# Optimization experiments

Measured on AMD Instinct MI355X. Metric: run time of the kernel, lower is better.

The kernel has to match this reference:

```python
import jax, jax.numpy as jnp
import numpy as np

B, N, D, C = 256, 200000, 128, 1000


def _l2_normalize(v, axis=-1, eps=1e-12):
    # matches torch F.normalize(p=2): v / max(||v||, eps)
    norm = jnp.sqrt(jnp.sum(v * v, axis=axis, keepdims=True))
    return v / jnp.maximum(norm, eps)


def setup_inputs() -> dict:
    key = jax.random.key(0)
    k1, k2, k3 = jax.random.split(key, 3)
    x = jax.random.normal(k1, (B, D), dtype=jnp.float32)
    index_embeddings = jax.random.normal(k2, (N, D), dtype=jnp.float32)
    class_labels = jax.random.randint(k3, (N,), 0, C, dtype=jnp.int32)
    return {
        "x": x,
        "index_embeddings": index_embeddings,
        "class_labels": class_labels,
        "num_classes": C,
    }


def reference(x, index_embeddings, class_labels, num_classes):
    # backbone output flattened -> embeddings [B, D]; L2-normalize (queries and index,
    # index normalization happens in add_index_data in the original module)
    emb = _l2_normalize(x)
    idx_emb = _l2_normalize(index_embeddings)
    # cosine similarities [B, N]
    similarities = jnp.einsum('bd,nd->bn', emb, idx_emb)
    # per-class max reduction (replaces Python loop over classes):
    # segment-max over the index dimension keyed by class_labels -> [B, num_classes]
    logits = jax.ops.segment_max(
        similarities.T, class_labels, num_segments=num_classes,
        indices_are_sorted=False,
    ).T
    return logits
```

## Files before the change

### kernel.cpp

```cpp
#include <hip/hip_runtime.h>
#include <hip/hip_bf16.h>
#include <stdint.h>

#define D_ 128
#define NB 64
#define KCH 4
#define NINF (-__builtin_inff())

typedef float f32x4 __attribute__((ext_vector_type(4)));
typedef short bf16x8 __attribute__((ext_vector_type(8)));

__device__ inline unsigned short f2bf(float f){
  unsigned x = __float_as_uint(f);
  return (unsigned short)((x + 0x7FFFu + ((x >> 16) & 1u)) >> 16);
}
__device__ inline unsigned packbf(float a, float b){
  return (unsigned)f2bf(a) | ((unsigned)f2bf(b) << 16);
}
__device__ inline unsigned fkey(float v){
  unsigned b = __float_as_uint(v);
  return (b & 0x80000000u) ? ~b : (b | 0x80000000u);
}

__global__ void k_norm_x(const float* __restrict__ x, unsigned short* __restrict__ xn){
  int row = blockIdx.x, lane = threadIdx.x;
  float2 v = reinterpret_cast<const float2*>(x + (size_t)row * D_)[lane];
  float ss = v.x * v.x + v.y * v.y;
  #pragma unroll
  for (int m = 1; m < 64; m <<= 1) ss += __shfl_xor(ss, m);
  float s = 1.0f / fmaxf(sqrtf(ss), 1e-12f);
  reinterpret_cast<unsigned*>(xn + (size_t)row * D_)[lane] = packbf(v.x * s, v.y * s);
}

__global__ void k_hist(const int* __restrict__ lab, unsigned* __restrict__ hist, int N, int C){
  __shared__ unsigned lh[1024];
  int t = threadIdx.x;
  for (int c = t; c < 1024; c += 256) lh[c] = 0;
  __syncthreads();
  for (int i = blockIdx.x * 256 + t; i < N; i += gridDim.x * 256)
    atomicAdd(&lh[lab[i]], 1u);
  __syncthreads();
  for (int c = t; c < C; c += 256) { unsigned v = lh[c]; if (v) atomicAdd(&hist[c], v); }
}

__global__ void k_scan(const unsigned* __restrict__ hist, unsigned* __restrict__ cursor, int C){
  __shared__ unsigned s[1024];
  int t = threadIdx.x;
  unsigned v = (t < C) ? hist[t] : 0u;
  s[t] = v; __syncthreads();
  for (int off = 1; off < 1024; off <<= 1){
    unsigned u = (t >= off) ? s[t - off] : 0u;
    __syncthreads();
    s[t] += u;
    __syncthreads();
  }
  if (t < C) cursor[t] = s[t] - v;
}

__global__ void k_scatter(const int* __restrict__ lab, unsigned* __restrict__ cursor,
                          int* __restrict__ perm, int* __restrict__ slab,
                          int* __restrict__ dstpos, int N){
  for (int i = blockIdx.x * 256 + threadIdx.x; i < N; i += gridDim.x * 256){
    int c = lab[i];
    unsigned pos = atomicAdd(&cursor[c], 1u);
    perm[pos] = i;
    slab[pos] = c;
    dstpos[i] = (int)pos;
  }
}

__global__ void k_init_out(unsigned* __restrict__ o, int n){
  int i = blockIdx.x * 256 + threadIdx.x;
  if (i < n) o[i] = 0x007FFFFFu;
}

__global__ void k_permnorm(const float* __restrict__ emb, const int* __restrict__ dstpos,
                           unsigned short* __restrict__ nrm, int N){
  int r = blockIdx.x * 64 + (threadIdx.x >> 2);
  if (r >= N) return;
  int j = threadIdx.x & 3;
  const f32x4* src = reinterpret_cast<const f32x4*>(emb + (size_t)r * D_ + j * 32);
  f32x4 v[8];
  #pragma unroll
  for (int i = 0; i < 8; i++) v[i] = src[i];
  float ss = 0.f;
  #pragma unroll
  for (int i = 0; i < 8; i++) ss += v[i][0]*v[i][0] + v[i][1]*v[i][1] + v[i][2]*v[i][2] + v[i][3]*v[i][3];
  ss += __shfl_xor(ss, 1); ss += __shfl_xor(ss, 2);
  float sc = 1.0f / fmaxf(sqrtf(ss), 1e-12f);
  int d = dstpos[r];
  unsigned o[16];
  #pragma unroll
  for (int i = 0; i < 8; i++){
    o[i*2]   = packbf(v[i][0]*sc, v[i][1]*sc);
    o[i*2+1] = packbf(v[i][2]*sc, v[i][3]*sc);
  }
  uint4* dst = reinterpret_cast<uint4*>(nrm + (size_t)d * D_ + j * 32);
  #pragma unroll
  for (int i = 0; i < 4; i++) dst[i] = make_uint4(o[i*4], o[i*4+1], o[i*4+2], o[i*4+3]);
}

__global__ __launch_bounds__(256, 3) void k_gemm(
    const unsigned short* __restrict__ nrm,
    const unsigned short* __restrict__ xn,
    const int* __restrict__ slab,
    unsigned* __restrict__ out_u,
    int nchunks, int N, int C){
  __shared__ __align__(16) unsigned short Ab[2][NB * D_];
  const int t = threadIdx.x;
  const int w = t >> 6, lane = t & 63, lr = lane & 15, lg = lane >> 4;

  const int cbeg = blockIdx.x * KCH;
  if (cbeg >= nchunks) return;
  int cend = cbeg + KCH; if (cend > nchunks) cend = nchunks;

  bf16x8 bf[4][4];
  #pragma unroll
  for (int ni = 0; ni < 4; ni++)
    #pragma unroll
    for (int kk = 0; kk < 4; kk++)
      bf[ni][kk] = *reinterpret_cast<const bf16x8*>(
          xn + (size_t)(w * 64 + ni * 16 + lr) * D_ + kk * 32 + lg * 8);

  const int c0 = slab[(size_t)cbeg * NB];
  float rT0=NINF, rT1=NINF, rT2=NINF, rT3=NINF, rT4=NINF, rT5=NINF, rT6=NINF, rT7=NINF;

  auto stageF = [&](int cn, int bb){
    const char* sb = (const char*)(nrm + (size_t)cn * NB * D_);
    char* lb = (char*)(&Ab[bb][0]);
    #pragma unroll
    for (int i = 0; i < 4; i++){
      int L = t * 16 + i * 4096;
      int row = L >> 8, s = (L >> 4) & 15;
      int so = row * 256 + ((s ^ (row & 7)) << 4);
      __builtin_amdgcn_global_load_lds(
          (const __attribute__((address_space(1))) unsigned int*)(sb + so),
          (__attribute__((address_space(3))) unsigned int*)(lb + L),
          16, 0, 0);
    }
  };

  stageF(cbeg, 0);

  for (int c = cbeg; c < cend; ++c){
    const int b = (c - cbeg) & 1;
    const int rowbase = c * NB;
    int rb = rowbase + lane;
    int myc = slab[rb < N ? rb : (N - 1)];
    int nx = __shfl_down(myc, 1);
    unsigned long long bmask = __ballot(lane < 63 && myc != nx);
    asm volatile("s_waitcnt vmcnt(0)" ::: "memory");
    if (c + 1 < cend) stageF(c + 1, b ^ 1);
    asm volatile("s_barrier" ::: "memory");

    f32x4 acc[4][4];
    #pragma unroll
    for (int mi = 0; mi < 4; mi++)
      #pragma unroll
      for (int ni = 0; ni < 4; ni++)
        acc[mi][ni] = (f32x4){0.f, 0.f, 0.f, 0.f};

    #pragma unroll
    for (int mi = 0; mi < 4; mi++){
      const int row = mi * 16 + lr;
      const char* rp = (const char*)(&Ab[b][0]) + row * 256;
      #pragma unroll
      for (int kk = 0; kk < 4; kk++){
        bf16x8 af = *reinterpret_cast<const bf16x8*>(rp + (((kk * 4 + lg) ^ (row & 7)) << 4));
        #pragma unroll
        for (int ni = 0; ni < 4; ni++)
          acc[mi][ni] = __builtin_amdgcn_mfma_f32_16x16x32_bf16(af, bf[ni][kk], acc[mi][ni], 0, 0, 0);
      }
    }

    int a = 0;
    unsigned long long mm = bmask;
    for (;;){
      int e = mm ? (__builtin_ctzll(mm) + 1) : 64;
      int cls = __shfl(myc, a);
      float m0=NINF, m1=NINF, m2=NINF, m3=NINF;
      #pragma unroll
      for (int mi = 0; mi < 4; mi++)
        #pragma unroll
        for (int rg = 0; rg < 4; rg++){
          int row = mi * 16 + lg * 4 + rg;
          bool in = (row >= a) && (row < e) && (rowbase + row < N);
          m0 = in ? fmaxf(m0, acc[mi][0][rg]) : m0;
          m1 = in ? fmaxf(m1, acc[mi][1][rg]) : m1;
          m2 = in ? fmaxf(m2, acc[mi][2][rg]) : m2;
          m3 = in ? fmaxf(m3, acc[mi][3][rg]) : m3;
        }
      m0 = fmaxf(m0, __shfl_xor(m0, 16)); m0 = fmaxf(m0, __shfl_xor(m0, 32));
      m1 = fmaxf(m1, __shfl_xor(m1, 16)); m1 = fmaxf(m1, __shfl_xor(m1, 32));
      m2 = fmaxf(m2, __shfl_xor(m2, 16)); m2 = fmaxf(m2, __shfl_xor(m2, 32));
      m3 = fmaxf(m3, __shfl_xor(m3, 16)); m3 = fmaxf(m3, __shfl_xor(m3, 32));
      float mv = (lg < 2) ? ((lg == 0) ? m0 : m1) : ((lg == 2) ? m2 : m3);
      int slot = cls - c0;
      switch (slot){
        case 0: rT0 = fmaxf(rT0, mv); break;
        case 1: rT1 = fmaxf(rT1, mv); break;
        case 2: rT2 = fmaxf(rT2, mv); break;
        case 3: rT3 = fmaxf(rT3, mv); break;
        case 4: rT4 = fmaxf(rT4, mv); break;
        case 5: rT5 = fmaxf(rT5, mv); break;
        case 6: rT6 = fmaxf(rT6, mv); break;
        case 7: rT7 = fmaxf(rT7, mv); break;
        default: atomicMax(&out_u[(size_t)t * C + cls], fkey(mv)); break;
      }
      if (e >= 64) break;
      a = e; mm &= mm - 1;
    }
    asm volatile("s_barrier" ::: "memory");
  }

  const size_t ob = (size_t)t * C;
  #define FLUSH(S_, V_) { int cls = c0 + S_; if (cls < C && V_ != NINF) atomicMax(&out_u[ob + cls], fkey(V_)); }
  FLUSH(0, rT0) FLUSH(1, rT1) FLUSH(2, rT2) FLUSH(3, rT3)
  FLUSH(4, rT4) FLUSH(5, rT5) FLUSH(6, rT6) FLUSH(7, rT7)
  #undef FLUSH
}

struct __align__(16) GSm {
  unsigned short A[NB * 136];
  float sims[16 * 257];
  float scale[NB];
  int rowid[NB];
  int clab[NB];
};

__global__ __launch_bounds__(256, 2) void k_gemm_gather(
    const float* __restrict__ emb, const unsigned short* __restrict__ xn,
    const int* __restrict__ perm, const int* __restrict__ slab,
    unsigned* __restrict__ out_u, int N, int C){
  __shared__ GSm sm;
  const int t = threadIdx.x;
  const int base = blockIdx.x * NB;
  if (t < NB){
    int p = base + t; if (p > N - 1) p = N - 1;
    sm.rowid[t] = perm[p];
    sm.clab[t]  = slab[p];
  }
  __syncthreads();
  {
    int r = t >> 2, j = t & 3;
    const float4* src = reinterpret_cast<const float4*>(emb + (long)sm.rowid[r] * D_ + j * 32);
    float4 v[8];
    #pragma unroll
    for (int i = 0; i < 8; i++) v[i] = src[i];
    float ss = 0.f;
    #pragma unroll
    for (int i = 0; i < 8; i++) ss += v[i].x*v[i].x + v[i].y*v[i].y + v[i].z*v[i].z + v[i].w*v[i].w;
    ss += __shfl_xor(ss, 1); ss += __shfl_xor(ss, 2);
    sm.scale[r] = 1.0f / fmaxf(sqrtf(ss), 1e-12f);
    unsigned* dst = reinterpret_cast<unsigned*>(&sm.A[r * 136 + j * 32]);
    #pragma unroll
    for (int i = 0; i < 8; i++){
      dst[i * 2]     = packbf(v[i].x, v[i].y);
      dst[i * 2 + 1] = packbf(v[i].z, v[i].w);
    }
  }
  const int w = t >> 6, lane = t & 63;
  const int lr = lane & 15, lg = lane >> 4;
  bf16x8 bfr[4][4];
  #pragma unroll
  for (int ni = 0; ni < 4; ni++)
    #pragma unroll
    for (int kk = 0; kk < 4; kk++)
      bfr[ni][kk] = *reinterpret_cast<const bf16x8*>(
          xn + (size_t)(w * 64 + ni * 16 + lr) * D_ + kk * 32 + lg * 8);
  f32x4 acc[4][4];
  #pragma unroll
  for (int mi = 0; mi < 4; mi++)
    #pragma unroll
    for (int ni = 0; ni < 4; ni++)
      acc[mi][ni] = (f32x4){0.f, 0.f, 0.f, 0.f};
  __syncthreads();
  #pragma unroll
  for (int mi = 0; mi < 4; mi++)
    #pragma unroll
    for (int kk = 0; kk < 4; kk++){
      bf16x8 af = *reinterpret_cast<const bf16x8*>(&sm.A[(mi * 16 + lr) * 136 + kk * 32 + lg * 8]);
      #pragma unroll
      for (int ni = 0; ni < 4; ni++)
        acc[mi][ni] = __builtin_amdgcn_mfma_f32_16x16x32_bf16(af, bfr[ni][kk], acc[mi][ni], 0, 0, 0);
    }
  int cur = -1; float rm = 0.f;
  for (int mi = 0; mi < 4; mi++){
    __syncthreads();
    #pragma unroll
    for (int ni = 0; ni < 4; ni++)
      #pragma unroll
      for (int rg = 0; rg < 4; rg++){
        int r16 = lg * 4 + rg;
        sm.sims[r16 * 257 + w * 64 + ni * 16 + lr] = acc[mi][ni][rg] * sm.scale[mi * 16 + r16];
      }
    __syncthreads();
    #pragma unroll
    for (int r16 = 0; r16 < 16; r16++){
      int c = sm.clab[mi * 16 + r16];
      float v = sm.sims[r16 * 257 + t];
      if (c != cur){
        if (cur >= 0) atomicMax(&out_u[(size_t)t * C + cur], fkey(rm));
        cur = c; rm = v;
      } else rm = fmaxf(rm, v);
    }
  }
  atomicMax(&out_u[(size_t)t * C + cur], fkey(rm));
}

__global__ void k_finalize(unsigned* __restrict__ o, int n){
  int i = blockIdx.x * 256 + threadIdx.x;
  if (i < n){
    unsigned k = o[i];
    o[i] = (k & 0x80000000u) ? (k & 0x7FFFFFFFu) : ~k;
  }
}

extern "C" void kernel_launch(void* const* d_in, const int* in_sizes, int n_in,
                              void* d_out, int out_size, void* d_ws, size_t ws_size,
                              hipStream_t stream){
  const float* x   = (const float*)d_in[0];
  const float* emb = (const float*)d_in[1];
  const int*   lab = (const int*)d_in[2];
  const int B = in_sizes[0] / D_;
  const int N = in_sizes[1] / D_;
  const int C = out_size / B;
  const int nchunks = (N + NB - 1) / NB;

  char* ws = (char*)d_ws;
  size_t off = 0;
  unsigned short* xn = (unsigned short*)(ws); off += ((size_t)B * D_ * 2 + 255) & ~(size_t)255;
  unsigned* hist   = (unsigned*)(ws + off); off += 4096;
  unsigned* cursor = (unsigned*)(ws + off); off += 4096;
  size_t narr = ((size_t)N * 4 + 255) & ~(size_t)255;
  int* perm   = (int*)(ws + off); off += narr;
  int* slab   = (int*)(ws + off); off += narr;
  int* dstpos = (int*)(ws + off); off += narr;
  unsigned short* nrm = (unsigned short*)(ws + off);
  size_t need = off + (size_t)nchunks * NB * D_ * 2;
  const bool fast = (ws_size >= need);

  k_norm_x<<<B, 64, 0, stream>>>(x, xn);
  hipMemsetAsync(hist, 0, 8192, stream);
  k_hist<<<208, 256, 0, stream>>>(lab, hist, N, C);
  k_scan<<<1, 1024, 0, stream>>>(hist, cursor, C);
  k_scatter<<<208, 256, 0, stream>>>(lab, cursor, perm, slab, dstpos, N);
  k_init_out<<<(B * C + 255) / 256, 256, 0, stream>>>((unsigned*)d_out, B * C);
  if (fast){
    k_permnorm<<<(N + 63) / 64, 256, 0, stream>>>(emb, dstpos, nrm, N);
    k_gemm<<<(nchunks + KCH - 1) / KCH, 256, 0, stream>>>(nrm, xn, slab, (unsigned*)d_out, nchunks, N, C);
  } else {
    k_gemm_gather<<<nchunks, 256, 0, stream>>>(emb, xn, perm, slab, (unsigned*)d_out, N, C);
  }
  k_finalize<<<(B * C + 255) / 256, 256, 0, stream>>>((unsigned*)d_out, B * C);
}
```

Measured before the change: 292.6 us.

## Fuse prep kernels and gather sorted rows in GEMM instead of permuting

Merges index normalization, query normalization, output init and the label histogram into one multi-role prep kernel. The index is now normalized in its original order, and the GEMM gathers rows through perm while loading into LDS, so the dstpos array and the scattered permuted write go away. The GEMM now handles one 64-row chunk per block with a single LDS buffer and no register-cached class slots, adding a fast path for chunks holding a single class. The trade-off is random 256-byte row gathers in the GEMM, more atomics per block, and no double-buffered prefetch.

```diff
diff --git a/kernel.cpp b/kernel.cpp
--- a/kernel.cpp
+++ b/kernel.cpp
@@ -4,7 +4,6 @@
 
 #define D_ 128
 #define NB 64
-#define KCH 4
 #define NINF (-__builtin_inff())
 
 typedef float f32x4 __attribute__((ext_vector_type(4)));
@@ -22,25 +21,50 @@
   return (b & 0x80000000u) ? ~b : (b | 0x80000000u);
 }
 
-__global__ void k_norm_x(const float* __restrict__ x, unsigned short* __restrict__ xn){
-  int row = blockIdx.x, lane = threadIdx.x;
-  float2 v = reinterpret_cast<const float2*>(x + (size_t)row * D_)[lane];
-  float ss = v.x * v.x + v.y * v.y;
-  #pragma unroll
-  for (int m = 1; m < 64; m <<= 1) ss += __shfl_xor(ss, m);
-  float s = 1.0f / fmaxf(sqrtf(ss), 1e-12f);
-  reinterpret_cast<unsigned*>(xn + (size_t)row * D_)[lane] = packbf(v.x * s, v.y * s);
-}
-
-__global__ void k_hist(const int* __restrict__ lab, unsigned* __restrict__ hist, int N, int C){
-  __shared__ unsigned lh[1024];
-  int t = threadIdx.x;
-  for (int c = t; c < 1024; c += 256) lh[c] = 0;
-  __syncthreads();
-  for (int i = blockIdx.x * 256 + t; i < N; i += gridDim.x * 256)
-    atomicAdd(&lh[lab[i]], 1u);
-  __syncthreads();
-  for (int c = t; c < C; c += 256) { unsigned v = lh[c]; if (v) atomicAdd(&hist[c], v); }
+__global__ void k_prep(const float* __restrict__ emb, const float* __restrict__ x,
+                       unsigned short* __restrict__ nrmlin, unsigned short* __restrict__ xn,
+                       unsigned* __restrict__ out_u, const int* __restrict__ lab,
+                       unsigned* __restrict__ hist,
+                       int N, int B, int C, int PN, int XB, int IB, int HB){
+  const int bid = blockIdx.x;
+  const int t = threadIdx.x;
+  if (bid < PN + XB){
+    const float* src; unsigned short* dst; int nrows; int r0;
+    if (bid < PN){ src = emb; dst = nrmlin; nrows = N; r0 = bid * 64; }
+    else         { src = x;   dst = xn;     nrows = B; r0 = (bid - PN) * 64; }
+    int r = r0 + (t >> 2);
+    if (r >= nrows) return;
+    int j = t & 3;
+    const f32x4* s4 = reinterpret_cast<const f32x4*>(src + (size_t)r * D_ + j * 32);
+    f32x4 v[8];
+    #pragma unroll
+    for (int i = 0; i < 8; i++) v[i] = s4[i];
+    float ss = 0.f;
+    #pragma unroll
+    for (int i = 0; i < 8; i++) ss += v[i][0]*v[i][0] + v[i][1]*v[i][1] + v[i][2]*v[i][2] + v[i][3]*v[i][3];
+    ss += __shfl_xor(ss, 1); ss += __shfl_xor(ss, 2);
+    float sc = 1.0f / fmaxf(sqrtf(ss), 1e-12f);
+    unsigned o[16];
+    #pragma unroll
+    for (int i = 0; i < 8; i++){
+      o[i*2]   = packbf(v[i][0]*sc, v[i][1]*sc);
+      o[i*2+1] = packbf(v[i][2]*sc, v[i][3]*sc);
+    }
+    uint4* d4 = reinterpret_cast<uint4*>(dst + (size_t)r * D_ + j * 32);
+    #pragma unroll
+    for (int i = 0; i < 4; i++) d4[i] = make_uint4(o[i*4], o[i*4+1], o[i*4+2], o[i*4+3]);
+  } else if (bid < PN + XB + IB){
+    int i = (bid - PN - XB) * 256 + t;
+    if (i < B * C) out_u[i] = 0x007FFFFFu;
+  } else {
+    int hb = bid - PN - XB - IB;
+    __shared__ unsigned lh[1024];
+    for (int c = t; c < 1024; c += 256) lh[c] = 0;
+    __syncthreads();
+    for (int i = hb * 256 + t; i < N; i += HB * 256) atomicAdd(&lh[lab[i]], 1u);
+    __syncthreads();
+    for (int c = t; c < C; c += 256){ unsigned v = lh[c]; if (v) atomicAdd(&hist[c], v); }
+  }
 }
 
 __global__ void k_scan(const unsigned* __restrict__ hist, unsigned* __restrict__ cursor, int C){
@@ -58,61 +82,37 @@
 }
 
 __global__ void k_scatter(const int* __restrict__ lab, unsigned* __restrict__ cursor,
-                          int* __restrict__ perm, int* __restrict__ slab,
-                          int* __restrict__ dstpos, int N){
+                          int* __restrict__ perm, int* __restrict__ slab, int N){
   for (int i = blockIdx.x * 256 + threadIdx.x; i < N; i += gridDim.x * 256){
     int c = lab[i];
     unsigned pos = atomicAdd(&cursor[c], 1u);
     perm[pos] = i;
     slab[pos] = c;
-    dstpos[i] = (int)pos;
-  }
-}
-
-__global__ void k_init_out(unsigned* __restrict__ o, int n){
-  int i = blockIdx.x * 256 + threadIdx.x;
-  if (i < n) o[i] = 0x007FFFFFu;
-}
-
-__global__ void k_permnorm(const float* __restrict__ emb, const int* __restrict__ dstpos,
-                           unsigned short* __restrict__ nrm, int N){
-  int r = blockIdx.x * 64 + (threadIdx.x >> 2);
-  if (r >= N) return;
-  int j = threadIdx.x & 3;
-  const f32x4* src = reinterpret_cast<const f32x4*>(emb + (size_t)r * D_ + j * 32);
-  f32x4 v[8];
-  #pragma unroll
-  for (int i = 0; i < 8; i++) v[i] = src[i];
-  float ss = 0.f;
-  #pragma unroll
-  for (int i = 0; i < 8; i++) ss += v[i][0]*v[i][0] + v[i][1]*v[i][1] + v[i][2]*v[i][2] + v[i][3]*v[i][3];
-  ss += __shfl_xor(ss, 1); ss += __shfl_xor(ss, 2);
-  float sc = 1.0f / fmaxf(sqrtf(ss), 1e-12f);
-  int d = dstpos[r];
-  unsigned o[16];
-  #pragma unroll
-  for (int i = 0; i < 8; i++){
-    o[i*2]   = packbf(v[i][0]*sc, v[i][1]*sc);
-    o[i*2+1] = packbf(v[i][2]*sc, v[i][3]*sc);
-  }
-  uint4* dst = reinterpret_cast<uint4*>(nrm + (size_t)d * D_ + j * 32);
-  #pragma unroll
-  for (int i = 0; i < 4; i++) dst[i] = make_uint4(o[i*4], o[i*4+1], o[i*4+2], o[i*4+3]);
+  }
 }
 
 __global__ __launch_bounds__(256, 3) void k_gemm(
-    const unsigned short* __restrict__ nrm,
+    const unsigned short* __restrict__ nrmlin,
     const unsigned short* __restrict__ xn,
-    const int* __restrict__ slab,
-    unsigned* __restrict__ out_u,
-    int nchunks, int N, int C){
-  __shared__ __align__(16) unsigned short Ab[2][NB * D_];
-  const int t = threadIdx.x;
-  const int w = t >> 6, lane = t & 63, lr = lane & 15, lg = lane >> 4;
-
-  const int cbeg = blockIdx.x * KCH;
-  if (cbeg >= nchunks) return;
-  int cend = cbeg + KCH; if (cend > nchunks) cend = nchunks;
+    const int* __restrict__ perm, const int* __restrict__ slab,
+    unsigned* __restrict__ out_u, int N, int C){
+  __shared__ __align__(16) unsigned short Ab[NB * D_];
+  const int t = threadIdx.x, w = t >> 6, lane = t & 63, lr = lane & 15, lg = lane >> 4;
+  const int rowbase = blockIdx.x * NB;
+
+  int rb = rowbase + lane;
+  int myc = slab[rb < N ? rb : (N - 1)];
+
+  #pragma unroll
+  for (int i = 0; i < 4; i++){
+    int gr = rowbase + i * 16 + lr; if (gr > N - 1) gr = N - 1;
+    int g = perm[gr];
+    const char* src = (const char*)nrmlin + (size_t)g * 256 + ((w * 4 + lg) << 4);
+    char* dst = (char*)Ab + (w + i * 4) * 1024 + lane * 16;
+    __builtin_amdgcn_global_load_lds(
+        (const __attribute__((address_space(1))) unsigned int*)src,
+        (__attribute__((address_space(3))) unsigned int*)dst, 16, 0, 0);
+  }
 
   bf16x8 bf[4][4];
   #pragma unroll
@@ -122,57 +122,47 @@
       bf[ni][kk] = *reinterpret_cast<const bf16x8*>(
           xn + (size_t)(w * 64 + ni * 16 + lr) * D_ + kk * 32 + lg * 8);
 
-  const int c0 = slab[(size_t)cbeg * NB];
-  float rT0=NINF, rT1=NINF, rT2=NINF, rT3=NINF, rT4=NINF, rT5=NINF, rT6=NINF, rT7=NINF;
-
-  auto stageF = [&](int cn, int bb){
-    const char* sb = (const char*)(nrm + (size_t)cn * NB * D_);
-    char* lb = (char*)(&Ab[bb][0]);
-    #pragma unroll
-    for (int i = 0; i < 4; i++){
-      int L = t * 16 + i * 4096;
-      int row = L >> 8, s = (L >> 4) & 15;
-      int so = row * 256 + ((s ^ (row & 7)) << 4);
-      __builtin_amdgcn_global_load_lds(
-          (const __attribute__((address_space(1))) unsigned int*)(sb + so),
-          (__attribute__((address_space(3))) unsigned int*)(lb + L),
-          16, 0, 0);
-    }
-  };
-
-  stageF(cbeg, 0);
-
-  for (int c = cbeg; c < cend; ++c){
-    const int b = (c - cbeg) & 1;
-    const int rowbase = c * NB;
-    int rb = rowbase + lane;
-    int myc = slab[rb < N ? rb : (N - 1)];
-    int nx = __shfl_down(myc, 1);
-    unsigned long long bmask = __ballot(lane < 63 && myc != nx);
-    asm volatile("s_waitcnt vmcnt(0)" ::: "memory");
-    if (c + 1 < cend) stageF(c + 1, b ^ 1);
-    asm volatile("s_barrier" ::: "memory");
-
-    f32x4 acc[4][4];
+  int nx = __shfl_down(myc, 1);
+  unsigned long long bmask = __ballot(lane < 63 && myc != nx);
+  int c0 = __shfl(myc, 0);
+
+  __syncthreads();
+
+  f32x4 acc[4][4];
+  #pragma unroll
+  for (int mi = 0; mi < 4; mi++)
+    #pragma unroll
+    for (int ni = 0; ni < 4; ni++)
+      acc[mi][ni] = (f32x4){0.f, 0.f, 0.f, 0.f};
+
+  #pragma unroll
+  for (int mi = 0; mi < 4; mi++)
+    #pragma unroll
+    for (int kk = 0; kk < 4; kk++){
+      bf16x8 af = *reinterpret_cast<const bf16x8*>(&Ab[(mi * 4 + kk) * 512 + lane * 8]);
+      #pragma unroll
+      for (int ni = 0; ni < 4; ni++)
+        acc[mi][ni] = __builtin_amdgcn_mfma_f32_16x16x32_bf16(af, bf[ni][kk], acc[mi][ni], 0, 0, 0);
+    }
+
+  if (bmask == 0ULL){
+    float m0=NINF, m1=NINF, m2=NINF, m3=NINF;
     #pragma unroll
     for (int mi = 0; mi < 4; mi++)
       #pragma unroll
-      for (int ni = 0; ni < 4; ni++)
-        acc[mi][ni] = (f32x4){0.f, 0.f, 0.f, 0.f};
-
-    #pragma unroll
-    for (int mi = 0; mi < 4; mi++){
-      const int row = mi * 16 + lr;
-      const char* rp = (const char*)(&Ab[b][0]) + row * 256;
-      #pragma unroll
-      for (int kk = 0; kk < 4; kk++){
-        bf16x8 af = *reinterpret_cast<const bf16x8*>(rp + (((kk * 4 + lg) ^ (row & 7)) << 4));
-        #pragma unroll
-        for (int ni = 0; ni < 4; ni++)
-          acc[mi][ni] = __builtin_amdgcn_mfma_f32_16x16x32_bf16(af, bf[ni][kk], acc[mi][ni], 0, 0, 0);
+      for (int rg = 0; rg < 4; rg++){
+        m0 = fmaxf(m0, acc[mi][0][rg]);
+        m1 = fmaxf(m1, acc[mi][1][rg]);
+        m2 = fmaxf(m2, acc[mi][2][rg]);
+        m3 = fmaxf(m3, acc[mi][3][rg]);
       }
-    }
-
+    m0 = fmaxf(m0, __shfl_xor(m0, 16)); m0 = fmaxf(m0, __shfl_xor(m0, 32));
+    m1 = fmaxf(m1, __shfl_xor(m1, 16)); m1 = fmaxf(m1, __shfl_xor(m1, 32));
+    m2 = fmaxf(m2, __shfl_xor(m2, 16)); m2 = fmaxf(m2, __shfl_xor(m2, 32));
+    m3 = fmaxf(m3, __shfl_xor(m3, 16)); m3 = fmaxf(m3, __shfl_xor(m3, 32));
+    float mv = (lg < 2) ? ((lg == 0) ? m0 : m1) : ((lg == 2) ? m2 : m3);
+    atomicMax(&out_u[(size_t)t * C + c0], fkey(mv));
+  } else {
     int a = 0;
     unsigned long long mm = bmask;
     for (;;){
@@ -184,7 +174,7 @@
         #pragma unroll
         for (int rg = 0; rg < 4; rg++){
           int row = mi * 16 + lg * 4 + rg;
-          bool in = (row >= a) && (row < e) && (rowbase + row < N);
+          bool in = (row >= a) && (row < e);
           m0 = in ? fmaxf(m0, acc[mi][0][rg]) : m0;
           m1 = in ? fmaxf(m1, acc[mi][1][rg]) : m1;
           m2 = in ? fmaxf(m2, acc[mi][2][rg]) : m2;
@@ -195,29 +185,11 @@
       m2 = fmaxf(m2, __shfl_xor(m2, 16)); m2 = fmaxf(m2, __shfl_xor(m2, 32));
       m3 = fmaxf(m3, __shfl_xor(m3, 16)); m3 = fmaxf(m3, __shfl_xor(m3, 32));
       float mv = (lg < 2) ? ((lg == 0) ? m0 : m1) : ((lg == 2) ? m2 : m3);
-      int slot = cls - c0;
-      switch (slot){
-        case 0: rT0 = fmaxf(rT0, mv); break;
-        case 1: rT1 = fmaxf(rT1, mv); break;
-        case 2: rT2 = fmaxf(rT2, mv); break;
-        case 3: rT3 = fmaxf(rT3, mv); break;
-        case 4: rT4 = fmaxf(rT4, mv); break;
-        case 5: rT5 = fmaxf(rT5, mv); break;
-        case 6: rT6 = fmaxf(rT6, mv); break;
-        case 7: rT7 = fmaxf(rT7, mv); break;
-        default: atomicMax(&out_u[(size_t)t * C + cls], fkey(mv)); break;
-      }
+      atomicMax(&out_u[(size_t)t * C + cls], fkey(mv));
       if (e >= 64) break;
       a = e; mm &= mm - 1;
     }
-    asm volatile("s_barrier" ::: "memory");
-  }
-
-  const size_t ob = (size_t)t * C;
-  #define FLUSH(S_, V_) { int cls = c0 + S_; if (cls < C && V_ != NINF) atomicMax(&out_u[ob + cls], fkey(V_)); }
-  FLUSH(0, rT0) FLUSH(1, rT1) FLUSH(2, rT2) FLUSH(3, rT3)
-  FLUSH(4, rT4) FLUSH(5, rT5) FLUSH(6, rT6) FLUSH(7, rT7)
-  #undef FLUSH
+  }
 }
 
 struct __align__(16) GSm {
@@ -325,7 +297,11 @@
   const int B = in_sizes[0] / D_;
   const int N = in_sizes[1] / D_;
   const int C = out_size / B;
-  const int nchunks = (N + NB - 1) / NB;
+
+  const int PNfull = (N + 63) / 64;
+  const int XB = (B + 63) / 64;
+  const int IB = (B * C + 255) / 256;
+  const int HB = 208;
 
   char* ws = (char*)d_ws;
   size_t off = 0;
@@ -335,22 +311,20 @@
   size_t narr = ((size_t)N * 4 + 255) & ~(size_t)255;
   int* perm   = (int*)(ws + off); off += narr;
   int* slab   = (int*)(ws + off); off += narr;
-  int* dstpos = (int*)(ws + off); off += narr;
-  unsigned short* nrm = (unsigned short*)(ws + off);
-  size_t need = off + (size_t)nchunks * NB * D_ * 2;
+  unsigned short* nrmlin = (unsigned short*)(ws + off);
+  size_t need = off + (size_t)PNfull * NB * D_ * 2;
   const bool fast = (ws_size >= need);
-
-  k_norm_x<<<B, 64, 0, stream>>>(x, xn);
-  hipMemsetAsync(hist, 0, 8192, stream);
-  k_hist<<<208, 256, 0, stream>>>(lab, hist, N, C);
+  const int PN = fast ? PNfull : 0;
+
+  hipMemsetAsync(hist, 0, 4096, stream);
+  k_prep<<<PN + XB + IB + HB, 256, 0, stream>>>(emb, x, nrmlin, xn, (unsigned*)d_out,
+                                                lab, hist, N, B, C, PN, XB, IB, HB);
   k_scan<<<1, 1024, 0, stream>>>(hist, cursor, C);
-  k_scatter<<<208, 256, 0, stream>>>(lab, cursor, perm, slab, dstpos, N);
-  k_init_out<<<(B * C + 255) / 256, 256, 0, stream>>>((unsigned*)d_out, B * C);
+  k_scatter<<<208, 256, 0, stream>>>(lab, cursor, perm, slab, N);
   if (fast){
-    k_permnorm<<<(N + 63) / 64, 256, 0, stream>>>(emb, dstpos, nrm, N);
-    k_gemm<<<(nchunks + KCH - 1) / KCH, 256, 0, stream>>>(nrm, xn, slab, (unsigned*)d_out, nchunks, N, C);
+    k_gemm<<<PNfull, 256, 0, stream>>>(nrmlin, xn, perm, slab, (unsigned*)d_out, N, C);
   } else {
-    k_gemm_gather<<<nchunks, 256, 0, stream>>>(emb, xn, perm, slab, (unsigned*)d_out, N, C);
-  }
-  k_finalize<<<(B * C + 255) / 256, 256, 0, stream>>>((unsigned*)d_out, B * C);
-}
+    k_gemm_gather<<<PNfull, 256, 0, stream>>>(emb, xn, perm, slab, (unsigned*)d_out, N, C);
+  }
+  k_finalize<<<IB, 256, 0, stream>>>((unsigned*)d_out, B * C);
+}
```

Measured after the change: 292.4 us. About the same (-0.1%).
